# Performance work log

Hardware: AMD Instinct MI355X
Metric: run time of the kernel (lower is better)

## Reference

```python
import jax, jax.numpy as jnp
import numpy as np

N_SRC = 200000
N_DST = 50000
N_EDGES = 800000
N_IN = 256
N_OUT = 128


def setup_inputs() -> dict:
    key = jax.random.key(0)
    ks = jax.random.split(key, 10)
    x = jax.random.normal(ks[0], (N_SRC, N_IN), dtype=jnp.float32)
    edge_rows = jax.random.randint(ks[1], (N_EDGES,), 0, N_DST, dtype=jnp.int32)
    edge_cols = jax.random.randint(ks[2], (N_EDGES,), 0, N_SRC, dtype=jnp.int32)
    edge_vals = jax.random.uniform(ks[3], (N_EDGES,), dtype=jnp.float32)
    sampled_nodes = jax.random.randint(ks[4], (N_DST,), 0, N_SRC, dtype=jnp.int32)
    W_w = jax.random.normal(ks[5], (N_IN, N_OUT), dtype=jnp.float32) * 0.05
    b_w = jax.random.normal(ks[6], (N_OUT,), dtype=jnp.float32) * 0.05
    W_b = jax.random.normal(ks[7], (N_IN, N_OUT), dtype=jnp.float32) * 0.05
    b_b = jax.random.normal(ks[8], (N_OUT,), dtype=jnp.float32) * 0.05
    scale = jnp.ones((2 * N_OUT,), dtype=jnp.float32)
    offset = jnp.zeros((2 * N_OUT,), dtype=jnp.float32)
    return {"x": x, "edge_rows": edge_rows, "edge_cols": edge_cols,
            "edge_vals": edge_vals, "sampled_nodes": sampled_nodes,
            "W_w": W_w, "b_w": b_w, "W_b": W_b, "b_b": b_b,
            "scale": scale, "offset": offset}


def reference(x, edge_rows, edge_cols, edge_vals, sampled_nodes,
              W_w, b_w, W_b, b_b, scale, offset):
    # SpMM: feat[r] = sum_e vals[e] * x[cols[e]] for rows[e]==r  -> [N_DST, N_IN]
    msgs = edge_vals[:, None] * x[edge_cols]
    feat = jax.ops.segment_sum(msgs, edge_rows, num_segments=N_DST)
    # dual linear + concat -> [N_DST, 2*N_OUT]
    self_part = x[sampled_nodes] @ W_b + b_b
    neigh_part = feat @ W_w + b_w
    out = jax.nn.elu(jnp.concatenate([self_part, neigh_part], axis=1))
    # row-wise normalize (biased variance), then affine
    mean = out.mean(axis=1, keepdims=True)
    var = out.var(axis=1, keepdims=True) + 1e-9
    return (out - mean) * scale * jax.lax.rsqrt(var) + offset
```

## Files before the change

### kernel.cpp

```cpp
#include <hip/hip_runtime.h>
#include <math.h>

#define N_SRC   200000
#define N_DST   50000
#define N_EDGES 800000
#define N_IN    256
#define N_OUT   128
#define CAP     64

#define WS_CNT   0
#define WS_WTW   204800
#define WS_WTB   270336
#define WS_SELF  335872
#define WS_Y     13135872
#define WS_CSR   64335872

typedef short  bf16x8 __attribute__((ext_vector_type(8)));
typedef unsigned short u16x8 __attribute__((ext_vector_type(8)));
typedef float  f32x4  __attribute__((ext_vector_type(4)));

__device__ inline unsigned short f2bf(float f) {
    unsigned u = __builtin_bit_cast(unsigned, f);
    u += 0x7fffu + ((u >> 16) & 1u);
    return (unsigned short)(u >> 16);
}
__device__ inline float bf2f(unsigned short h) {
    return __builtin_bit_cast(float, (unsigned)h << 16);
}

__global__ __launch_bounds__(256) void k_init(const float* __restrict__ Ww,
                                              const float* __restrict__ Wb,
                                              unsigned short* __restrict__ Wtw,
                                              unsigned short* __restrict__ Wtb,
                                              int* __restrict__ cnt) {
    int tot = blockIdx.x * 256 + threadIdx.x;
    int sel = tot >> 15;
    int idx = tot & 32767;
    int n = idx >> 8, k = idx & 255;
    const float* src = sel ? Wb : Ww;
    unsigned short* dst = sel ? Wtb : Wtw;
    dst[n * 256 + k] = f2bf(src[k * 128 + n]);
    if (tot < N_DST) cnt[tot] = 0;
}

#define GSCAT 3125
#define GBIG  3125
#define GSELF 782
#define LDA 40
#define EPS 132

__global__ __launch_bounds__(256, 8) void k_mega(
        const float* __restrict__ x,
        const int* __restrict__ erows, const int* __restrict__ ecols,
        const float* __restrict__ evals, const int* __restrict__ sn,
        const unsigned short* __restrict__ Wtw, const unsigned short* __restrict__ Wtb,
        int* __restrict__ cnt, int2* __restrict__ csr_pad,
        unsigned short* __restrict__ ybuf, unsigned short* __restrict__ selfp) {
    __shared__ __align__(16) unsigned short sm[8448];
    unsigned short* smA = sm;
    unsigned short* smB = sm + 2560;
    const int tid = threadIdx.x;

    if (blockIdx.x < GSCAT) {
        int i = blockIdx.x * 256 + tid;
        int r = erows[i];
        int rank = atomicAdd(&cnt[r], 1);
        if (rank < CAP) {
            int2 cv;
            cv.x = ecols[i];
            cv.y = __builtin_bit_cast(int, evals[i]);
            csr_pad[r * CAP + rank] = cv;
        }
        return;
    }

    const int gb = blockIdx.x - GSCAT;
    const bool isBig = gb < GBIG;
    const int* rowidx = isBig ? nullptr : sn;
    const unsigned short* Bt = isBig ? Wtw : Wtb;
    unsigned short* Y = isBig ? ybuf : selfp;
    const int M = isBig ? N_SRC : N_DST;
    const int bid = isBig ? gb : gb - GBIG;

    const int lane = tid & 63, wid = tid >> 6;
    const int l15 = lane & 15, quad = lane >> 4;
    const int row0 = bid * 64;

    const int ar = tid >> 2, aseg = (tid & 3) * 8;
    int srow = row0 + ar;
    if (srow >= M) srow = M - 1;
    if (rowidx) srow = rowidx[srow];
    const float* aptr = x + (long)srow * 256 + aseg;
    const int bn = tid >> 1, bh = (tid & 1) * 16;
    const unsigned short* bptr = Bt + (long)bn * 256 + bh;

    unsigned short* smAw = &smA[ar * LDA + aseg];
    unsigned short* smBw = &smB[bn * LDA + bh];
    const unsigned short* smAr = &smA[(wid * 16 + l15) * LDA + quad * 8];

    f32x4 acc[8];
    #pragma unroll
    for (int t = 0; t < 8; t++) acc[t] = (f32x4){0.f, 0.f, 0.f, 0.f};

    for (int kt = 0; kt < 8; kt++) {
        const int k0 = kt * 32;
        {
            const float4* s4 = (const float4*)(aptr + k0);
            float4 v0 = s4[0], v1 = s4[1];
            u16x8 w;
            w[0]=f2bf(v0.x); w[1]=f2bf(v0.y); w[2]=f2bf(v0.z); w[3]=f2bf(v0.w);
            w[4]=f2bf(v1.x); w[5]=f2bf(v1.y); w[6]=f2bf(v1.z); w[7]=f2bf(v1.w);
            *(u16x8*)smAw = w;
        }
        {
            const u16x8* s8 = (const u16x8*)(bptr + k0);
            u16x8 b0 = s8[0], b1 = s8[1];
            *(u16x8*)smBw       = b0;
            *(u16x8*)(smBw + 8) = b1;
        }
        __syncthreads();
        bf16x8 af = *(const bf16x8*)smAr;
        #pragma unroll
        for (int t = 0; t < 8; t++) {
            bf16x8 bfv = *(const bf16x8*)&smB[(t * 16 + l15) * LDA + quad * 8];
            acc[t] = __builtin_amdgcn_mfma_f32_16x16x32_bf16(af, bfv, acc[t], 0, 0, 0);
        }
        __syncthreads();
    }

    #pragma unroll
    for (int t = 0; t < 8; t++)
        #pragma unroll
        for (int rg = 0; rg < 4; rg++)
            sm[(wid * 16 + quad * 4 + rg) * EPS + t * 16 + l15] = f2bf(acc[t][rg]);
    __syncthreads();
    const int orow = tid >> 2, oc0 = (tid & 3) * 32;
    if (row0 + orow < M) {
        unsigned short* dst = Y + (long)(row0 + orow) * 128 + oc0;
        #pragma unroll
        for (int i = 0; i < 4; i++)
            *(u16x8*)(dst + i * 8) = *(const u16x8*)&sm[orow * EPS + oc0 + i * 8];
    }
}

#define GATHER(j) \
    int   c##j = __shfl(cv.x, e0 + j, 64); \
    float v##j = __builtin_bit_cast(float, __shfl(cv.y, e0 + j, 64)); \
    unsigned p##j = *(const unsigned*)(y + (long)c##j * 128 + (lane << 1));
#define ACCUM(j) \
    a0 = fmaf(v##j, __builtin_bit_cast(float, p##j << 16), a0); \
    a1 = fmaf(v##j, __builtin_bit_cast(float, p##j & 0xffff0000u), a1);

__global__ __launch_bounds__(256) void k_sage(const unsigned short* __restrict__ y,
                                              const unsigned short* __restrict__ selfp,
                                              const int* __restrict__ cnt,
                                              const int2* __restrict__ csr_pad,
                                              const float* __restrict__ bw,
                                              const float* __restrict__ bb,
                                              const float* __restrict__ scale,
                                              const float* __restrict__ offs,
                                              float* __restrict__ out) {
    const int tid = threadIdx.x, lane = tid & 63, wid = tid >> 6;
    const int row = blockIdx.x * 4 + wid;
    const int m = min(cnt[row], CAP);

    int2 cv = (lane < m) ? csr_pad[(long)row * CAP + lane] : make_int2(0, 0);

    unsigned spk = *(const unsigned*)(selfp + (long)row * 128 + lane * 2);
    float s0 = bf2f((unsigned short)(spk & 0xffff)) + bb[lane * 2];
    float s1 = bf2f((unsigned short)(spk >> 16))    + bb[lane * 2 + 1];
    s0 = s0 > 0.f ? s0 : expm1f(s0);
    s1 = s1 > 0.f ? s1 : expm1f(s1);

    float a0 = 0.f, a1 = 0.f;
    const int mm = (m + 7) & ~7;
    for (int e0 = 0; e0 < mm; e0 += 8) {
        GATHER(0) GATHER(1) GATHER(2) GATHER(3)
        GATHER(4) GATHER(5) GATHER(6) GATHER(7)
        ACCUM(0) ACCUM(1) ACCUM(2) ACCUM(3)
        ACCUM(4) ACCUM(5) ACCUM(6) ACCUM(7)
    }
    a0 += bw[lane * 2];
    a1 += bw[lane * 2 + 1];
    a0 = a0 > 0.f ? a0 : expm1f(a0);
    a1 = a1 > 0.f ? a1 : expm1f(a1);

    float s  = s0 + s1 + a0 + a1;
    float s2 = s0 * s0 + s1 * s1 + a0 * a0 + a1 * a1;
    #pragma unroll
    for (int o = 32; o > 0; o >>= 1) {
        s  += __shfl_xor(s,  o, 64);
        s2 += __shfl_xor(s2, o, 64);
    }
    float mean = s * (1.f / 256.f);
    float var  = s2 * (1.f / 256.f) - mean * mean;
    float rstd = rsqrtf(var + 1e-9f);

    float* orow = out + (long)row * 256;
    float2 w0, w1;
    w0.x = (s0 - mean) * rstd * scale[lane * 2]           + offs[lane * 2];
    w0.y = (s1 - mean) * rstd * scale[lane * 2 + 1]       + offs[lane * 2 + 1];
    w1.x = (a0 - mean) * rstd * scale[128 + lane * 2]     + offs[128 + lane * 2];
    w1.y = (a1 - mean) * rstd * scale[128 + lane * 2 + 1] + offs[128 + lane * 2 + 1];
    *(float2*)(orow + lane * 2)       = w0;
    *(float2*)(orow + 128 + lane * 2) = w1;
}

extern "C" void kernel_launch(void* const* d_in, const int* in_sizes, int n_in,
                              void* d_out, int out_size, void* d_ws, size_t ws_size,
                              hipStream_t stream) {
    const float* x     = (const float*)d_in[0];
    const int*   erows = (const int*)  d_in[1];
    const int*   ecols = (const int*)  d_in[2];
    const float* evals = (const float*)d_in[3];
    const int*   sn    = (const int*)  d_in[4];
    const float* Ww    = (const float*)d_in[5];
    const float* bw    = (const float*)d_in[6];
    const float* Wb    = (const float*)d_in[7];
    const float* bb    = (const float*)d_in[8];
    const float* scale = (const float*)d_in[9];
    const float* offs  = (const float*)d_in[10];
    float* out = (float*)d_out;

    char* ws = (char*)d_ws;
    int*   cnt     = (int*)  (ws + WS_CNT);
    unsigned short* Wtw   = (unsigned short*)(ws + WS_WTW);
    unsigned short* Wtb   = (unsigned short*)(ws + WS_WTB);
    unsigned short* selfp = (unsigned short*)(ws + WS_SELF);
    unsigned short* ybuf  = (unsigned short*)(ws + WS_Y);
    int2*  csr_pad = (int2*) (ws + WS_CSR);

    k_init <<<256, 256, 0, stream>>>(Ww, Wb, Wtw, Wtb, cnt);
    k_mega <<<GSCAT + GBIG + GSELF, 256, 0, stream>>>(x, erows, ecols, evals, sn,
                                                      Wtw, Wtb, cnt, csr_pad, ybuf, selfp);
    k_sage <<<N_DST / 4, 256, 0, stream>>>(ybuf, selfp, cnt, csr_pad,
                                           bw, bb, scale, offs, out);
}
```

Measured before the change: 421.1 us.

## Load MFMA operands directly from global memory, drop LDS staging in GEMM

The projection GEMM no longer stages A and B tiles through shared memory with two barriers per k-step. Each lane now loads its own A fragment (fp32 converted to bf16) and its B fragments straight from global or cache into registers, and the k-loop is fully unrolled. Occupancy hint drops from 8 to 4 blocks to allow more registers. This removes the sync and LDS traffic but has each wave re-read the full B matrix from cache, raising register pressure and L2 traffic.

```diff
diff --git a/kernel.cpp b/kernel.cpp
--- a/kernel.cpp
+++ b/kernel.cpp
@@ -46,19 +46,16 @@
 #define GSCAT 3125
 #define GBIG  3125
 #define GSELF 782
-#define LDA 40
 #define EPS 132
 
-__global__ __launch_bounds__(256, 8) void k_mega(
+__global__ __launch_bounds__(256, 4) void k_mega(
         const float* __restrict__ x,
         const int* __restrict__ erows, const int* __restrict__ ecols,
         const float* __restrict__ evals, const int* __restrict__ sn,
         const unsigned short* __restrict__ Wtw, const unsigned short* __restrict__ Wtb,
         int* __restrict__ cnt, int2* __restrict__ csr_pad,
         unsigned short* __restrict__ ybuf, unsigned short* __restrict__ selfp) {
-    __shared__ __align__(16) unsigned short sm[8448];
-    unsigned short* smA = sm;
-    unsigned short* smB = sm + 2560;
+    __shared__ __align__(16) unsigned short sm[64 * EPS];
     const int tid = threadIdx.x;
 
     if (blockIdx.x < GSCAT) {
@@ -86,46 +83,33 @@
     const int l15 = lane & 15, quad = lane >> 4;
     const int row0 = bid * 64;
 
-    const int ar = tid >> 2, aseg = (tid & 3) * 8;
-    int srow = row0 + ar;
+    int srow = row0 + wid * 16 + l15;
     if (srow >= M) srow = M - 1;
     if (rowidx) srow = rowidx[srow];
-    const float* aptr = x + (long)srow * 256 + aseg;
-    const int bn = tid >> 1, bh = (tid & 1) * 16;
-    const unsigned short* bptr = Bt + (long)bn * 256 + bh;
-
-    unsigned short* smAw = &smA[ar * LDA + aseg];
-    unsigned short* smBw = &smB[bn * LDA + bh];
-    const unsigned short* smAr = &smA[(wid * 16 + l15) * LDA + quad * 8];
+    const float*          ap = x  + (long)srow * 256 + quad * 8;
+    const unsigned short* bp = Bt + (long)l15 * 256 + quad * 8;
 
     f32x4 acc[8];
     #pragma unroll
     for (int t = 0; t < 8; t++) acc[t] = (f32x4){0.f, 0.f, 0.f, 0.f};
 
+    #pragma unroll
     for (int kt = 0; kt < 8; kt++) {
         const int k0 = kt * 32;
-        {
-            const float4* s4 = (const float4*)(aptr + k0);
-            float4 v0 = s4[0], v1 = s4[1];
-            u16x8 w;
-            w[0]=f2bf(v0.x); w[1]=f2bf(v0.y); w[2]=f2bf(v0.z); w[3]=f2bf(v0.w);
-            w[4]=f2bf(v1.x); w[5]=f2bf(v1.y); w[6]=f2bf(v1.z); w[7]=f2bf(v1.w);
-            *(u16x8*)smAw = w;
-        }
-        {
-            const u16x8* s8 = (const u16x8*)(bptr + k0);
-            u16x8 b0 = s8[0], b1 = s8[1];
-            *(u16x8*)smBw       = b0;
-            *(u16x8*)(smBw + 8) = b1;
-        }
-        __syncthreads();
-        bf16x8 af = *(const bf16x8*)smAr;
-        #pragma unroll
-        for (int t = 0; t < 8; t++) {
-            bf16x8 bfv = *(const bf16x8*)&smB[(t * 16 + l15) * LDA + quad * 8];
-            acc[t] = __builtin_amdgcn_mfma_f32_16x16x32_bf16(af, bfv, acc[t], 0, 0, 0);
-        }
-        __syncthreads();
+        float4 a0 = *(const float4*)(ap + k0);
+        float4 a1 = *(const float4*)(ap + k0 + 4);
+        bf16x8 bfr[8];
+        #pragma unroll
+        for (int t = 0; t < 8; t++)
+            bfr[t] = *(const bf16x8*)(bp + (long)t * 4096 + k0);
+        bf16x8 af;
+        af[0] = (short)f2bf(a0.x); af[1] = (short)f2bf(a0.y);
+        af[2] = (short)f2bf(a0.z); af[3] = (short)f2bf(a0.w);
+        af[4] = (short)f2bf(a1.x); af[5] = (short)f2bf(a1.y);
+        af[6] = (short)f2bf(a1.z); af[7] = (short)f2bf(a1.w);
+        #pragma unroll
+        for (int t = 0; t < 8; t++)
+            acc[t] = __builtin_amdgcn_mfma_f32_16x16x32_bf16(af, bfr[t], acc[t], 0, 0, 0);
     }
 
     #pragma unroll
```

Result: slower. 489.1 us (+16.2%).
